# Optimization experiments

Hardware: AMD Instinct MI355X
Metric: run time of the kernel (lower is better)

## Reference

```python
import jax, jax.numpy as jnp
import numpy as np


def setup_inputs() -> dict:
    key = jax.random.key(0)
    ks = jax.random.split(key, 12)
    B, C, H, W = 8, 512, 48, 48
    HW = H * W
    inp = {
        'key': jax.random.normal(ks[0], (B, C, H, W), dtype=jnp.float32),
        'sds': jax.random.uniform(ks[1], (B, HW, H, W), dtype=jnp.float32),
        'global_bg': jax.random.normal(ks[2], (B, HW, C), dtype=jnp.float32),
        'global_fg': jax.random.normal(ks[3], (B, HW, C), dtype=jnp.float32),
        'local_bg': jax.random.normal(ks[4], (B, HW, C), dtype=jnp.float32),
        'local_fg': jax.random.normal(ks[5], (B, HW, C), dtype=jnp.float32),
        'overall_bg': jax.random.normal(ks[6], (B, 1, C), dtype=jnp.float32),
        'overall_fg': jax.random.normal(ks[7], (B, 1, C), dtype=jnp.float32),
        'short_bg': jax.random.normal(ks[8], (B, 1, C), dtype=jnp.float32),
        'short_fg': jax.random.normal(ks[9], (B, 1, C), dtype=jnp.float32),
        'long_bg': jax.random.normal(ks[10], (B, 1, C), dtype=jnp.float32),
        'long_fg': jax.random.normal(ks[11], (B, 1, C), dtype=jnp.float32),
    }
    return inp


def reference(key, sds, global_bg, global_fg, local_bg, local_fg,
              overall_bg, overall_fg, short_bg, short_fg, long_bg, long_fg):
    B, C, H, W = key.shape
    HW = H * W
    k = key.reshape(B, C, HW)                 # [B, C, HW]
    mask = sds.reshape(B, HW, HW)             # [B, HW(mem), HW(query)]

    def fine_max(bank, m=None):
        # bank: [B, HW, C]; score: [B, HW(mem), HW(query)]
        s = jnp.einsum('bmc,bcn->bmn', bank, k)
        if m is not None:
            s = s * m
        return jnp.max(s, axis=1).reshape(B, 1, H, W)

    def coarse(bank):
        # bank: [B, 1, C]
        return jnp.einsum('boc,bcn->bon', bank, k).reshape(B, 1, H, W)

    global_score = jnp.concatenate([fine_max(global_bg), fine_max(global_fg)], axis=1)
    local_score = jnp.concatenate([fine_max(local_bg, mask), fine_max(local_fg, mask)], axis=1)
    fine_score = jnp.concatenate([global_score, local_score], axis=1)

    coarse_score = jnp.concatenate([
        coarse(overall_bg), coarse(overall_fg),
        coarse(short_bg), coarse(short_fg),
        coarse(long_bg), coarse(long_fg),
    ], axis=1)

    matching_score = jnp.concatenate([fine_score, coarse_score], axis=1)  # [B, 10, H, W]
    return matching_score
```

## Files before the change

kernel.cpp:

```cpp
#include <hip/hip_runtime.h>

#define B_   8
#define C_   512
#define HW_  2304
#define BM   128
#define BN   128
#define BK   64
#define NT_  (HW_ / BN)
#define MT_PER_BLOCK 3
#define MCHUNKS 6

typedef __bf16 bf16x8 __attribute__((ext_vector_type(8)));
typedef float  f32x4  __attribute__((ext_vector_type(4)));

__device__ __forceinline__ unsigned short f2bf(float f) {
  unsigned int u = __float_as_uint(f);
  u += 0x7FFF + ((u >> 16) & 1);
  return (unsigned short)(u >> 16);
}

__device__ __forceinline__ void gload_lds16(const void* g, void* l) {
  __builtin_amdgcn_global_load_lds(
      (const __attribute__((address_space(1))) unsigned int*)g,
      (__attribute__((address_space(3))) unsigned int*)l, 16, 0, 0);
}

__global__ void zero_out(float* __restrict__ out, int n) {
  int i = blockIdx.x * 256 + threadIdx.x;
  if (i < n) out[i] = 0.0f;
}

__global__ void transpose_coarse(const float* __restrict__ key,
                                 const float* __restrict__ v0, const float* __restrict__ v1,
                                 const float* __restrict__ v2, const float* __restrict__ v3,
                                 const float* __restrict__ v4, const float* __restrict__ v5,
                                 unsigned short* __restrict__ keyT,
                                 float* __restrict__ out) {
  __shared__ float tile[32][33];
  __shared__ float red2[6][8][32];
  int b  = blockIdx.z;
  int n0 = blockIdx.x * 32;
  int c0 = blockIdx.y * 32;
  int tx = threadIdx.x;
  int ty = threadIdx.y;
#pragma unroll
  for (int i = 0; i < 4; i++) {
    int c = c0 + ty + i * 8;
    tile[ty + i * 8][tx] = key[(size_t)b * C_ * HW_ + (size_t)c * HW_ + n0 + tx];
  }
  __syncthreads();
#pragma unroll
  for (int i = 0; i < 4; i++) {
    int n = n0 + ty + i * 8;
    keyT[(size_t)b * HW_ * C_ + (size_t)n * C_ + c0 + tx] = f2bf(tile[tx][ty + i * 8]);
  }
  float s[6] = {0.f, 0.f, 0.f, 0.f, 0.f, 0.f};
#pragma unroll
  for (int i = 0; i < 4; i++) {
    int cr = ty * 4 + i;
    int c  = c0 + cr;
    float kv = tile[cr][tx];
    s[0] += v0[b * C_ + c] * kv;
    s[1] += v1[b * C_ + c] * kv;
    s[2] += v2[b * C_ + c] * kv;
    s[3] += v3[b * C_ + c] * kv;
    s[4] += v4[b * C_ + c] * kv;
    s[5] += v5[b * C_ + c] * kv;
  }
#pragma unroll
  for (int j = 0; j < 6; j++) red2[j][ty][tx] = s[j];
  __syncthreads();
  if (ty < 6) {
    float a = 0.f;
#pragma unroll
    for (int k = 0; k < 8; k++) a += red2[ty][k][tx];
    atomicAdd(&out[((size_t)b * 10 + 4 + ty) * HW_ + n0 + tx], a);
  }
}

__global__ void convert_banks(const float* __restrict__ b0, const float* __restrict__ b1,
                              const float* __restrict__ b2, const float* __restrict__ b3,
                              unsigned short* __restrict__ out) {
  const size_t per = (size_t)B_ * HW_ * C_;
  int g = blockIdx.y;
  const float* src = (g == 0) ? b0 : (g == 1) ? b1 : (g == 2) ? b2 : b3;
  size_t i = ((size_t)blockIdx.x * blockDim.x + threadIdx.x) * 4;
  float4 v = *(const float4*)(src + i);
  ushort4 o;
  o.x = f2bf(v.x); o.y = f2bf(v.y); o.z = f2bf(v.z); o.w = f2bf(v.w);
  *(ushort4*)(out + g * per + i) = o;
}

__global__ __launch_bounds__(256, 3) void fine_kernel(
    const unsigned short* __restrict__ keyT,
    const unsigned short* __restrict__ banks,
    const float* __restrict__ sds,
    float* __restrict__ pmax) {
  int nt = blockIdx.x % NT_;
  int mc = blockIdx.x / NT_;
  int gp = blockIdx.y;
  int b  = blockIdx.z;
  int n0 = nt * BN;

  __shared__ __align__(16) unsigned short A0[BM * 64];
  __shared__ __align__(16) unsigned short A1[BM * 64];
  __shared__ __align__(16) unsigned short Bl[BN * 64];
  __shared__ float red[4 * BN];

  int t    = threadIdx.x;
  int wave = t >> 6;
  int lane = t & 63;
  int quad = lane >> 4;
  int l15  = lane & 15;
  int wm   = (wave & 1) * 64;
  int wn   = (wave >> 1) * 64;

  int srow = lane >> 3;
  int ssub = (lane & 7) ^ srow;
  int l7  = l15 & 7;
  int sw0 = ((quad) ^ l7) * 8;
  int sw1 = ((quad + 4) ^ l7) * 8;

  const unsigned short* bank0 = banks + ((size_t)(2 * gp) * B_ + b) * (size_t)HW_ * C_;
  const unsigned short* bank1 = banks + ((size_t)(2 * gp + 1) * B_ + b) * (size_t)HW_ * C_;
  const unsigned short* keyb  = keyT + (size_t)b * HW_ * C_;
  const float* maskb = sds + (size_t)b * HW_ * HW_;
  const bool masked = (gp == 1);

  float rm0[4], rm1[4];
#pragma unroll
  for (int i = 0; i < 4; i++) { rm0[i] = -3.4e38f; rm1[i] = -3.4e38f; }

  for (int mi = 0; mi < MT_PER_BLOCK; mi++) {
    int m0 = (mc * MT_PER_BLOCK + mi) * BM;
    f32x4 acc0[4][4], acc1[4][4];
#pragma unroll
    for (int i = 0; i < 4; i++)
#pragma unroll
      for (int j = 0; j < 4; j++)
#pragma unroll
        for (int e = 0; e < 4; e++) { acc0[i][j][e] = 0.0f; acc1[i][j][e] = 0.0f; }

    for (int kc = 0; kc < C_ / BK; kc++) {
      __syncthreads();
#pragma unroll
      for (int j = 0; j < 4; j++) {
        int rbase = wave * 32 + j * 8;
        int row   = rbase + srow;
        size_t goff = (size_t)row * C_ + kc * BK + ssub * 8;
        gload_lds16(bank0 + (size_t)m0 * C_ + goff, &A0[rbase * 64]);
        gload_lds16(bank1 + (size_t)m0 * C_ + goff, &A1[rbase * 64]);
        gload_lds16(keyb  + (size_t)n0 * C_ + goff, &Bl[rbase * 64]);
      }
      __syncthreads();
#pragma unroll
      for (int k0 = 0; k0 < BK; k0 += 32) {
        int sw = (k0 == 0) ? sw0 : sw1;
        bf16x8 a0[4], a1[4], bb[4];
#pragma unroll
        for (int ms = 0; ms < 4; ms++) {
          a0[ms] = *(const bf16x8*)(&A0[(wm + ms * 16 + l15) * 64 + sw]);
          a1[ms] = *(const bf16x8*)(&A1[(wm + ms * 16 + l15) * 64 + sw]);
        }
#pragma unroll
        for (int ns = 0; ns < 4; ns++)
          bb[ns] = *(const bf16x8*)(&Bl[(wn + ns * 16 + l15) * 64 + sw]);
#pragma unroll
        for (int ms = 0; ms < 4; ms++)
#pragma unroll
          for (int ns = 0; ns < 4; ns++) {
            acc0[ms][ns] = __builtin_amdgcn_mfma_f32_16x16x32_bf16(
                a0[ms], bb[ns], acc0[ms][ns], 0, 0, 0);
            acc1[ms][ns] = __builtin_amdgcn_mfma_f32_16x16x32_bf16(
                a1[ms], bb[ns], acc1[ms][ns], 0, 0, 0);
          }
      }
    }

#pragma unroll
    for (int ms = 0; ms < 4; ms++) {
#pragma unroll
      for (int ns = 0; ns < 4; ns++) {
        int n = n0 + wn + ns * 16 + l15;
#pragma unroll
        for (int r = 0; r < 4; r++) {
          int m = m0 + wm + ms * 16 + quad * 4 + r;
          float s0 = acc0[ms][ns][r];
          float s1 = acc1[ms][ns][r];
          if (masked) {
            float w = maskb[(size_t)m * HW_ + n];
            s0 *= w; s1 *= w;
          }
          rm0[ns] = fmaxf(rm0[ns], s0);
          rm1[ns] = fmaxf(rm1[ns], s1);
        }
      }
    }
  }

#pragma unroll
  for (int ns = 0; ns < 4; ns++) {
    float v = rm0[ns];
    v = fmaxf(v, __shfl_xor(v, 16, 64));
    v = fmaxf(v, __shfl_xor(v, 32, 64));
    rm0[ns] = v;
    float u = rm1[ns];
    u = fmaxf(u, __shfl_xor(u, 16, 64));
    u = fmaxf(u, __shfl_xor(u, 32, 64));
    rm1[ns] = u;
  }
  if (lane < 16) {
#pragma unroll
    for (int ns = 0; ns < 4; ns++) {
      red[(wave & 1) * BN + wn + ns * 16 + l15]           = rm0[ns];
      red[2 * BN + (wave & 1) * BN + wn + ns * 16 + l15]  = rm1[ns];
    }
  }
  __syncthreads();
  if (t < BN) {
    float vv0 = fmaxf(red[t], red[BN + t]);
    float vv1 = fmaxf(red[2 * BN + t], red[3 * BN + t]);
    pmax[(((size_t)mc * B_ + b) * 4 + 2 * gp)     * HW_ + n0 + t] = vv0;
    pmax[(((size_t)mc * B_ + b) * 4 + 2 * gp + 1) * HW_ + n0 + t] = vv1;
  }
}

__global__ void fine_combine(const float* __restrict__ pmax, float* __restrict__ out) {
  int i = blockIdx.x * 256 + threadIdx.x;
  if (i >= B_ * 4 * HW_) return;
  int n = i % HW_;
  int g = (i / HW_) % 4;
  int b = i / (HW_ * 4);
  float v = -3.4e38f;
#pragma unroll
  for (int mc = 0; mc < MCHUNKS; mc++)
    v = fmaxf(v, pmax[(((size_t)mc * B_ + b) * 4 + g) * HW_ + n]);
  out[((size_t)b * 10 + g) * HW_ + n] = v;
}

extern "C" void kernel_launch(void* const* d_in, const int* in_sizes, int n_in,
                              void* d_out, int out_size, void* d_ws, size_t ws_size,
                              hipStream_t stream) {
  const float* key  = (const float*)d_in[0];
  const float* sds  = (const float*)d_in[1];
  const float* gbg  = (const float*)d_in[2];
  const float* gfg  = (const float*)d_in[3];
  const float* lbg  = (const float*)d_in[4];
  const float* lfg  = (const float*)d_in[5];
  const float* obg  = (const float*)d_in[6];
  const float* ofg  = (const float*)d_in[7];
  const float* sbg  = (const float*)d_in[8];
  const float* sfg  = (const float*)d_in[9];
  const float* lobg = (const float*)d_in[10];
  const float* lofg = (const float*)d_in[11];
  float* out = (float*)d_out;

  unsigned short* keyT  = (unsigned short*)d_ws;
  unsigned short* banks = keyT + (size_t)B_ * HW_ * C_;
  float* pmax = (float*)(banks + (size_t)4 * B_ * HW_ * C_);

  zero_out<<<(out_size + 255) / 256, 256, 0, stream>>>(out, out_size);
  convert_banks<<<dim3((B_ * HW_ * C_) / (4 * 256), 4), 256, 0, stream>>>(gbg, gfg, lbg, lfg, banks);
  transpose_coarse<<<dim3(HW_ / 32, C_ / 32, B_), dim3(32, 8), 0, stream>>>(
      key, obg, ofg, sbg, sfg, lobg, lofg, keyT, out);
  fine_kernel<<<dim3(NT_ * MCHUNKS, 2, B_), 256, 0, stream>>>(keyT, banks, sds, pmax);
  fine_combine<<<(B_ * 4 * HW_ + 255) / 256, 256, 0, stream>>>(pmax, out);
}
```

Measured before the change: 723.0 us.

## Double-buffer LDS staging with smaller K slices and reorder block mapping

Splits the K dimension into 32-wide slices and double-buffers the A0/A1/B tiles in shared memory, so the next slice (or the first slice of the next M tile) is loaded asynchronously while MFMAs run on the current one. This removes one barrier per step and hides global-load latency. The grid is flattened and the batch index is taken from the low bits, so concurrently running blocks are spread across batches. It also changes the LDS swizzle for the narrower tile. Smaller K steps mean more barriers per tile, and the loads issued right after the barrier have no explicit wait, so correctness depends on the barrier waiting for outstanding LDS-DMA.

```diff
diff --git a/kernel.cpp b/kernel.cpp
--- a/kernel.cpp
+++ b/kernel.cpp
@@ -5,7 +5,8 @@
 #define HW_  2304
 #define BM   128
 #define BN   128
-#define BK   64
+#define BKQ  32
+#define NKS  (C_ / BKQ)
 #define NT_  (HW_ / BN)
 #define MT_PER_BLOCK 3
 #define MCHUNKS 6
@@ -96,15 +97,16 @@
     const unsigned short* __restrict__ banks,
     const float* __restrict__ sds,
     float* __restrict__ pmax) {
-  int nt = blockIdx.x % NT_;
-  int mc = blockIdx.x / NT_;
-  int gp = blockIdx.y;
-  int b  = blockIdx.z;
-  int n0 = nt * BN;
-
-  __shared__ __align__(16) unsigned short A0[BM * 64];
-  __shared__ __align__(16) unsigned short A1[BM * 64];
-  __shared__ __align__(16) unsigned short Bl[BN * 64];
+  int lin = blockIdx.x;
+  int b   = lin & 7;
+  int ix  = lin >> 3;
+  int gp  = (ix >= 108) ? 1 : 0;
+  int w   = ix - gp * 108;
+  int mc  = w / NT_;
+  int nt  = w % NT_;
+  int n0  = nt * BN;
+
+  __shared__ __align__(16) unsigned short sbuf[2][3][BM * BKQ];
   __shared__ float red[4 * BN];
 
   int t    = threadIdx.x;
@@ -115,11 +117,8 @@
   int wm   = (wave & 1) * 64;
   int wn   = (wave >> 1) * 64;
 
-  int srow = lane >> 3;
-  int ssub = (lane & 7) ^ srow;
-  int l7  = l15 & 7;
-  int sw0 = ((quad) ^ l7) * 8;
-  int sw1 = ((quad + 4) ^ l7) * 8;
+  int ksub = (lane & 3) ^ ((lane >> 3) & 3);
+  int swo  = (quad ^ ((l15 >> 1) & 3)) * 8;
 
   const unsigned short* bank0 = banks + ((size_t)(2 * gp) * B_ + b) * (size_t)HW_ * C_;
   const unsigned short* bank1 = banks + ((size_t)(2 * gp + 1) * B_ + b) * (size_t)HW_ * C_;
@@ -127,9 +126,26 @@
   const float* maskb = sds + (size_t)b * HW_ * HW_;
   const bool masked = (gp == 1);
 
+  auto STAGE = [&](int buf, int m0s, int kc) {
+    unsigned short* A0d = &sbuf[buf][0][0];
+    unsigned short* A1d = &sbuf[buf][1][0];
+    unsigned short* Bd  = &sbuf[buf][2][0];
+#pragma unroll
+    for (int j = 0; j < 2; j++) {
+      int rbase = j * 64 + wave * 16;
+      size_t go = (size_t)(rbase + (lane >> 2)) * C_ + (size_t)kc * BKQ + ksub * 8;
+      gload_lds16(bank0 + (size_t)m0s * C_ + go, &A0d[rbase * BKQ]);
+      gload_lds16(bank1 + (size_t)m0s * C_ + go, &A1d[rbase * BKQ]);
+      gload_lds16(keyb  + (size_t)n0  * C_ + go, &Bd [rbase * BKQ]);
+    }
+  };
+
   float rm0[4], rm1[4];
 #pragma unroll
   for (int i = 0; i < 4; i++) { rm0[i] = -3.4e38f; rm1[i] = -3.4e38f; }
+
+  int cur = 0;
+  STAGE(0, mc * MT_PER_BLOCK * BM, 0);
 
   for (int mi = 0; mi < MT_PER_BLOCK; mi++) {
     int m0 = (mc * MT_PER_BLOCK + mi) * BM;
@@ -141,40 +157,33 @@
 #pragma unroll
         for (int e = 0; e < 4; e++) { acc0[i][j][e] = 0.0f; acc1[i][j][e] = 0.0f; }
 
-    for (int kc = 0; kc < C_ / BK; kc++) {
+    for (int kc = 0; kc < NKS; kc++) {
       __syncthreads();
-#pragma unroll
-      for (int j = 0; j < 4; j++) {
-        int rbase = wave * 32 + j * 8;
-        int row   = rbase + srow;
-        size_t goff = (size_t)row * C_ + kc * BK + ssub * 8;
-        gload_lds16(bank0 + (size_t)m0 * C_ + goff, &A0[rbase * 64]);
-        gload_lds16(bank1 + (size_t)m0 * C_ + goff, &A1[rbase * 64]);
-        gload_lds16(keyb  + (size_t)n0 * C_ + goff, &Bl[rbase * 64]);
+      if (kc + 1 < NKS)                STAGE(cur ^ 1, m0, kc + 1);
+      else if (mi + 1 < MT_PER_BLOCK)  STAGE(cur ^ 1, m0 + BM, 0);
+
+      const unsigned short* A0s = &sbuf[cur][0][0];
+      const unsigned short* A1s = &sbuf[cur][1][0];
+      const unsigned short* Bs  = &sbuf[cur][2][0];
+      bf16x8 a0[4], a1[4], bb[4];
+#pragma unroll
+      for (int ms = 0; ms < 4; ms++) {
+        a0[ms] = *(const bf16x8*)(&A0s[(wm + ms * 16 + l15) * BKQ + swo]);
+        a1[ms] = *(const bf16x8*)(&A1s[(wm + ms * 16 + l15) * BKQ + swo]);
       }
-      __syncthreads();
-#pragma unroll
-      for (int k0 = 0; k0 < BK; k0 += 32) {
-        int sw = (k0 == 0) ? sw0 : sw1;
-        bf16x8 a0[4], a1[4], bb[4];
-#pragma unroll
-        for (int ms = 0; ms < 4; ms++) {
-          a0[ms] = *(const bf16x8*)(&A0[(wm + ms * 16 + l15) * 64 + sw]);
-          a1[ms] = *(const bf16x8*)(&A1[(wm + ms * 16 + l15) * 64 + sw]);
+#pragma unroll
+      for (int ns = 0; ns < 4; ns++)
+        bb[ns] = *(const bf16x8*)(&Bs[(wn + ns * 16 + l15) * BKQ + swo]);
+#pragma unroll
+      for (int ms = 0; ms < 4; ms++)
+#pragma unroll
+        for (int ns = 0; ns < 4; ns++) {
+          acc0[ms][ns] = __builtin_amdgcn_mfma_f32_16x16x32_bf16(
+              a0[ms], bb[ns], acc0[ms][ns], 0, 0, 0);
+          acc1[ms][ns] = __builtin_amdgcn_mfma_f32_16x16x32_bf16(
+              a1[ms], bb[ns], acc1[ms][ns], 0, 0, 0);
         }
-#pragma unroll
-        for (int ns = 0; ns < 4; ns++)
-          bb[ns] = *(const bf16x8*)(&Bl[(wn + ns * 16 + l15) * 64 + sw]);
-#pragma unroll
-        for (int ms = 0; ms < 4; ms++)
-#pragma unroll
-          for (int ns = 0; ns < 4; ns++) {
-            acc0[ms][ns] = __builtin_amdgcn_mfma_f32_16x16x32_bf16(
-                a0[ms], bb[ns], acc0[ms][ns], 0, 0, 0);
-            acc1[ms][ns] = __builtin_amdgcn_mfma_f32_16x16x32_bf16(
-                a1[ms], bb[ns], acc1[ms][ns], 0, 0, 0);
-          }
-      }
+      cur ^= 1;
     }
 
 #pragma unroll
@@ -188,8 +197,8 @@
           float s0 = acc0[ms][ns][r];
           float s1 = acc1[ms][ns][r];
           if (masked) {
-            float w = maskb[(size_t)m * HW_ + n];
-            s0 *= w; s1 *= w;
+            float w_ = maskb[(size_t)m * HW_ + n];
+            s0 *= w_; s1 *= w_;
           }
           rm0[ns] = fmaxf(rm0[ns], s0);
           rm1[ns] = fmaxf(rm1[ns], s1);
@@ -263,6 +272,6 @@
   convert_banks<<<dim3((B_ * HW_ * C_) / (4 * 256), 4), 256, 0, stream>>>(gbg, gfg, lbg, lfg, banks);
   transpose_coarse<<<dim3(HW_ / 32, C_ / 32, B_), dim3(32, 8), 0, stream>>>(
       key, obg, ofg, sbg, sfg, lobg, lofg, keyT, out);
-  fine_kernel<<<dim3(NT_ * MCHUNKS, 2, B_), 256, 0, stream>>>(keyT, banks, sds, pmax);
+  fine_kernel<<<dim3(NT_ * MCHUNKS * 2 * B_), 256, 0, stream>>>(keyT, banks, sds, pmax);
   fine_combine<<<(B_ * 4 * HW_ + 255) / 256, 256, 0, stream>>>(pmax, out);
 }
```

Result: no change. 734.2 us (+1.5%).
